# Performance work log

Hardware: AMD Instinct MI355X
Metric: run time of the kernel (lower is better)

## Reference

```python
import jax, jax.numpy as jnp
import numpy as np

N, E, G = 50000, 1600000, 512
IN_DIM, HEADS, C1, C2, HIDDEN = 128, 3, 32, 32, 512
NEG_SLOPE = 0.2
EPS = 1e-16


def _glorot(key, shape):
    fan_in = shape[0]
    return jax.random.normal(key, shape, dtype=jnp.float32) / np.sqrt(fan_in)


def setup_inputs() -> dict:
    key = jax.random.key(0)
    ks = jax.random.split(key, 16)
    x = jax.random.normal(ks[0], (N, IN_DIM), dtype=jnp.float32)
    edge_index = jax.random.randint(ks[1], (2, E), 0, N, dtype=jnp.int64)
    batch = (jnp.arange(N, dtype=jnp.int64) * G) // N  # sorted, all graphs non-empty
    d1, d2 = HEADS * C1, HEADS * C2
    return {
        "x": x,
        "W_l1": _glorot(ks[2], (IN_DIM, d1)), "b_l1": jnp.zeros((d1,), jnp.float32),
        "W_r1": _glorot(ks[3], (IN_DIM, d1)), "b_r1": jnp.zeros((d1,), jnp.float32),
        "att1": _glorot(ks[4], (HEADS, C1)), "bias1": jnp.zeros((d1,), jnp.float32),
        "W_l2": _glorot(ks[5], (d1, d2)), "b_l2": jnp.zeros((d2,), jnp.float32),
        "W_r2": _glorot(ks[6], (d1, d2)), "b_r2": jnp.zeros((d2,), jnp.float32),
        "att2": _glorot(ks[7], (HEADS, C2)), "bias2": jnp.zeros((d2,), jnp.float32),
        "W_fc1": _glorot(ks[8], (d1 + d2, HIDDEN)), "b_fc1": jnp.zeros((HIDDEN,), jnp.float32),
        "W_fc2": _glorot(ks[9], (HIDDEN, 2)), "b_fc2": jnp.zeros((2,), jnp.float32),
        "edge_index": edge_index,
        "batch": batch,
    }


def gatv2_conv(xin, src, dst, W_l, b_l, W_r, b_r, att, bias, heads, out_c):
    n = xin.shape[0]
    x_l = (xin @ W_l + b_l).reshape(n, heads, out_c)  # source-side projection
    x_r = (xin @ W_r + b_r).reshape(n, heads, out_c)  # target-side projection
    e = jax.nn.leaky_relu(x_l[src] + x_r[dst], NEG_SLOPE)  # [E', H, C]
    logits = jnp.einsum("ehc,hc->eh", e, att)  # [E', H]
    m = jax.ops.segment_max(logits, dst, num_segments=n)
    a = jnp.exp(logits - m[dst])
    denom = jax.ops.segment_sum(a, dst, num_segments=n)
    alpha = a / (denom[dst] + EPS)  # per-destination edge softmax (PyG semantics)
    out = jax.ops.segment_sum(x_l[src] * alpha[:, :, None], dst, num_segments=n)
    return out.reshape(n, heads * out_c) + bias


def reference(x, W_l1, b_l1, W_r1, b_r1, att1, bias1,
              W_l2, b_l2, W_r2, b_r2, att2, bias2,
              W_fc1, b_fc1, W_fc2, b_fc2, edge_index, batch):
    n = x.shape[0]
    loop = jnp.arange(n, dtype=edge_index.dtype)
    src = jnp.concatenate([edge_index[0], loop])  # PyG GATv2Conv adds self-loops
    dst = jnp.concatenate([edge_index[1], loop])
    h1 = jnp.tanh(gatv2_conv(x, src, dst, W_l1, b_l1, W_r1, b_r1, att1, bias1, HEADS, C1))
    h2 = jnp.tanh(gatv2_conv(h1, src, dst, W_l2, b_l2, W_r2, b_r2, att2, bias2, HEADS, C2))
    h = jnp.concatenate([h1, h2], axis=1)  # [N, (C1+C2)*H]
    first_idx = jnp.searchsorted(batch, jnp.arange(G, dtype=batch.dtype))  # first node of each graph
    pooled = h[first_idx]  # [G, (C1+C2)*H]
    hidden = jax.nn.relu(pooled @ W_fc1 + b_fc1)
    logits = hidden @ W_fc2 + b_fc2
    return jax.nn.log_softmax(logits, axis=1)
```

## Files before the change

kernel.cpp:

```cpp
#include <hip/hip_runtime.h>
#include <hip/hip_bf16.h>
#include <hip/hip_fp16.h>
#include <math.h>

#define NN 50000
#define EE 1600000
#define GG 512
#define INDIM 128
#define HEADS 3
#define CC 32
#define DD 96
#define HID 512
#define NEG 0.2f
#define NEGM1 (NEG - 1.0f)
#define EPS_DEN 1e-16f
#define CAP 128
#define NBW 1568
#define LOG2E 1.44269504f
#define PCLAMP2 86.5617f

#define PS_BL1   0
#define PS_BR1   96
#define PS_ATT1  192
#define PS_BIAS1 288
#define PS_BL2   384
#define PS_BR2   480
#define PS_ATT2  576
#define PS_BIAS2 672
#define PS_BFC1  768
#define PS_WFC2  1280
#define PS_BFC2  2304
#define PS_TOTAL 2308

typedef _Float16 h8 __attribute__((ext_vector_type(8)));
typedef float f4 __attribute__((ext_vector_type(4)));

static __device__ __forceinline__ float bf2f(__hip_bfloat16 v) { return __bfloat162float(v); }

static __device__ __forceinline__ int getI(const void* p, long long i, bool w64) {
    return w64 ? ((const int*)p)[2 * i] : ((const int*)p)[i];
}

static __device__ __forceinline__ float rawf(const void* p, int i, bool isbf) {
    return isbf ? bf2f(((const __hip_bfloat16*)p)[i]) : ((const float*)p)[i];
}

static __device__ __forceinline__ void load4(const void* p, int base, int e0, bool w64, int* v) {
    const int4* q = (const int4*)p;
    if (w64) {
        int4 a = q[(base + e0) >> 1];
        int4 b = q[((base + e0) >> 1) + 1];
        v[0] = a.x; v[1] = a.z; v[2] = b.x; v[3] = b.z;
    } else {
        int4 a = q[(base + e0) >> 2];
        v[0] = a.x; v[1] = a.y; v[2] = a.z; v[3] = a.w;
    }
}

static __device__ __forceinline__ bool testbit(const unsigned* b, int i) {
    return (b[i >> 5] >> (i & 31)) & 1u;
}

template <int CTRL>
static __device__ __forceinline__ float dpp_add(float v) {
    int t = __builtin_amdgcn_update_dpp(0, __float_as_int(v), CTRL, 0xF, 0xF, true);
    return v + __int_as_float(t);
}
static __device__ __forceinline__ float red16(float p) {
    p = dpp_add<0x121>(p);
    p = dpp_add<0x122>(p);
    p = dpp_add<0x124>(p);
    p = dpp_add<0x128>(p);
    return p;
}

static __device__ __forceinline__ float edge_e(float2 x, float2 xr2, float2 aa) {
    float t0 = x.x + xr2.x; t0 = fmaf(fminf(t0, 0.0f), NEGM1, t0);
    float t1 = x.y + xr2.y; t1 = fmaf(fminf(t1, 0.0f), NEGM1, t1);
    return exp2f(fminf(red16(fmaf(t1, aa.y, t0 * aa.x)), PCLAMP2));
}

__global__ void detect_kernel(const void* __restrict__ x, const void* __restrict__ ei,
                              int* __restrict__ flags)
{
    __shared__ int wild, zcnt;
    if (threadIdx.x == 0) { wild = 0; zcnt = 0; }
    __syncthreads();
    int w = 0, z = 0;
    const __hip_bfloat16* xb = (const __hip_bfloat16*)x;
    for (int i = threadIdx.x; i < 4096; i += 256) {
        float v = bf2f(xb[i]);
        if (!(fabsf(v) <= 1e6f)) w++;
    }
    const int* e32 = (const int*)ei;
    for (int i = threadIdx.x; i < 4096; i += 256) {
        if (e32[2 * i + 1] == 0) z++;
    }
    atomicAdd(&wild, w);
    atomicAdd(&zcnt, z);
    __syncthreads();
    if (threadIdx.x == 0) {
        flags[0] = (wild < 64) ? 1 : 0;
        flags[1] = (zcnt > 4000) ? 1 : 0;
    }
}

struct SetupArgs {
    const void *wl1, *wr1, *wl2, *wr2, *wfc1;
    const void *bl1, *br1, *att1, *bias1, *bl2, *br2, *att2, *bias2, *bfc1, *wfc2, *bfc2;
    const void *batch;
};

__global__ void setup_kernel(SetupArgs a, const int* __restrict__ flags,
                             float* __restrict__ P, __half* __restrict__ B1,
                             __half* __restrict__ B2, __half* __restrict__ Bfc,
                             int* __restrict__ deg, int* __restrict__ needed,
                             int* __restrict__ first, unsigned* __restrict__ pb,
                             int* __restrict__ cnt)
{
    const int task = blockIdx.y;
    const int idx = blockIdx.x * 256 + threadIdx.x;
    const bool isbf = flags[0] != 0;

    if (task == 0) {
        if (idx == 0) *cnt = 0;
        if (idx >= PS_TOTAL) return;
        const void* src; int rel;
        if (idx < 768) {
            int k = idx / 96; rel = idx - k * 96;
            const void* s8[8] = {a.bl1, a.br1, a.att1, a.bias1, a.bl2, a.br2, a.att2, a.bias2};
            src = s8[k];
        } else if (idx < 1280) { src = a.bfc1; rel = idx - 768; }
        else if (idx < 2304)   { src = a.wfc2; rel = idx - 1280; }
        else if (idx < 2306)   { src = a.bfc2; rel = idx - 2304; }
        else return;
        P[idx] = rawf(src, rel, isbf);
    } else if (task == 1 || task == 2) {
        const int KC = (task == 1) ? 4 : 3;
        const int total = 12 * KC * 64;
        if (idx >= total) return;
        int lane = idx & 63, t = idx >> 6;
        int kc = t % KC, ntile = t / KC;
        int n = ntile * 16 + (lane & 15);
        int kbase = kc * 32 + (lane >> 4) * 8;
        const void* W = (task == 1) ? (n < 96 ? a.wl1 : a.wr1) : (n < 96 ? a.wl2 : a.wr2);
        int n2 = (n < 96) ? n : n - 96;
        __half* dst = ((task == 1) ? B1 : B2) + (size_t)idx * 8;
#pragma unroll
        for (int j = 0; j < 8; j++) dst[j] = __float2half(rawf(W, (kbase + j) * 96 + n2, isbf));
    } else if (task == 3) {
        const int total = 32 * 6 * 64;
        if (idx >= total) return;
        int lane = idx & 63, t = idx >> 6;
        int kc = t % 6, ntile = t / 6;
        int n = ntile * 16 + (lane & 15);
        int kbase = kc * 32 + (lane >> 4) * 8;
        __half* dst = Bfc + (size_t)idx * 8;
#pragma unroll
        for (int j = 0; j < 8; j++) dst[j] = __float2half(rawf(a.wfc1, (kbase + j) * HID + n, isbf));
    } else if (task == 4) {
        int i0 = idx * 4;
#pragma unroll
        for (int j = 0; j < 4; j++) if (i0 + j < NN) deg[i0 + j] = 0;
    } else if (task == 5) {
        if (idx >= NN) return;
        const bool w64 = flags[1] != 0;
        int b = getI(a.batch, idx, w64);
        bool isf = (idx == 0) || (getI(a.batch, idx - 1, w64) != b);
        needed[idx] = isf ? 1 : 0;
        if (isf) first[b] = idx;
    } else {
        if (idx >= NBW) return;
        const bool w64 = flags[1] != 0;
        unsigned word = 0;
        int prev = (idx == 0) ? -1 : getI(a.batch, idx * 32 - 1, w64);
        for (int bit = 0; bit < 32; bit++) {
            int i = idx * 32 + bit;
            if (i >= NN) break;
            int b = getI(a.batch, i, w64);
            if (i == 0 || b != prev) word |= (1u << bit);
            prev = b;
        }
        pb[idx] = word;
    }
}

__global__ void mark_needed_kernel(const void* __restrict__ ei, const int* __restrict__ flags,
                                   const unsigned* __restrict__ pb, int* __restrict__ needed)
{
    int e0 = (blockIdx.x * 256 + threadIdx.x) * 4;
    if (e0 >= EE) return;
    const bool w64 = flags[1] != 0;
    int d4[4];
    load4(ei, EE, e0, w64, d4);
#pragma unroll
    for (int j = 0; j < 4; j++)
        if (testbit(pb, d4[j])) needed[getI(ei, e0 + j, w64)] = 1;
}

__global__ void scatter_compact_kernel(const void* __restrict__ ei, const int* __restrict__ flags,
                                       const int* __restrict__ needed,
                                       int* __restrict__ deg, int* __restrict__ csr,
                                       int* __restrict__ list, int* __restrict__ cnt)
{
    if (blockIdx.y == 1) {
        int i = blockIdx.x * 256 + threadIdx.x;
        if (i >= NN) return;
        if (needed[i]) list[atomicAdd(cnt, 1)] = i;
        return;
    }
    int e0 = (blockIdx.x * 256 + threadIdx.x) * 4;
    if (e0 >= EE) return;
    const bool w64 = flags[1] != 0;
    int s4[4], d4[4];
    load4(ei, EE, e0, w64, d4);
    int nd0 = needed[d4[0]], nd1 = needed[d4[1]], nd2 = needed[d4[2]], nd3 = needed[d4[3]];
    if (!(nd0 | nd1 | nd2 | nd3)) return;
    load4(ei, 0, e0, w64, s4);
    int nd[4] = {nd0, nd1, nd2, nd3};
#pragma unroll
    for (int j = 0; j < 4; j++) {
        int dst = d4[j];
        if (!nd[j]) continue;
        int pos = atomicAdd(&deg[dst], 1);
        if (pos < CAP) csr[(size_t)dst * CAP + pos] = s4[j] * (DD / 2);
    }
}

template <int KDIM, int MODE>
__global__ __launch_bounds__(256) void proj_mfma_kernel(
    const void* __restrict__ Ain, const __half* __restrict__ Bswz,
    const int* __restrict__ list, const int* __restrict__ cnt,
    const float* __restrict__ P, const int* __restrict__ flags, int offBl, int offBr,
    __half* __restrict__ xl, float* __restrict__ xr)
{
    constexpr int KC = KDIM / 32;
    __shared__ __half Bs[12 * KC * 64 * 8];
    const int tid = threadIdx.x;
    const int limit = MODE ? *cnt : NN;
    const int blockBase = blockIdx.x * 64;
    if (blockBase >= limit) return;

    {
        const int chunks = 12 * KC * 64;
        for (int i = tid; i < chunks; i += 256)
            reinterpret_cast<f4*>(Bs)[i] = reinterpret_cast<const f4*>(Bswz)[i];
    }
    __syncthreads();

    const int wave = tid >> 6;
    const int lane = tid & 63;
    const int base = blockBase + wave * 16;
    if (base >= limit) return;

    const int q = lane >> 4;
    const int mlane = lane & 15;

    int aIdx = base + mlane;
    int aRow;
    if (MODE) aRow = (aIdx < limit) ? list[aIdx] : list[limit - 1];
    else      aRow = (aIdx < limit) ? aIdx : 0;

    h8 a[KC];
    if (MODE == 1) {
        const h8* arow = reinterpret_cast<const h8*>((const __half*)Ain + (size_t)aRow * KDIM);
#pragma unroll
        for (int kc = 0; kc < KC; kc++) a[kc] = arow[kc * 4 + q];
    } else if (flags[0]) {
        const int4* arow = reinterpret_cast<const int4*>((const ushort*)Ain + (size_t)aRow * KDIM);
#pragma unroll
        for (int kc = 0; kc < KC; kc++) {
            int4 r = arow[kc * 4 + q];
            int ws[4] = {r.x, r.y, r.z, r.w};
#pragma unroll
            for (int i = 0; i < 4; i++) {
                a[kc][2 * i]     = (_Float16)__int_as_float(ws[i] << 16);
                a[kc][2 * i + 1] = (_Float16)__int_as_float(ws[i] & 0xffff0000);
            }
        }
    } else {
        const f4* arow = reinterpret_cast<const f4*>((const float*)Ain + (size_t)aRow * KDIM);
#pragma unroll
        for (int kc = 0; kc < KC; kc++) {
            f4 r0 = arow[kc * 8 + q * 2];
            f4 r1 = arow[kc * 8 + q * 2 + 1];
#pragma unroll
            for (int i = 0; i < 4; i++) {
                a[kc][i]     = (_Float16)r0[i];
                a[kc][4 + i] = (_Float16)r1[i];
            }
        }
    }

    int sRow[4];
#pragma unroll
    for (int r = 0; r < 4; r++) {
        int si = base + q * 4 + r;
        sRow[r] = (si < limit) ? (MODE ? list[si] : si) : -1;
    }

    const h8* Bf = reinterpret_cast<const h8*>(Bs);
#pragma unroll
    for (int ntile = 0; ntile < 12; ntile++) {
        int n = ntile * 16 + mlane;
        float bv = (n < 96) ? P[offBl + n] : P[offBr + n - 96];
        f4 acc = {bv, bv, bv, bv};
#pragma unroll
        for (int kc = 0; kc < KC; kc++) {
            h8 b = Bf[(ntile * KC + kc) * 64 + lane];
            acc = __builtin_amdgcn_mfma_f32_16x16x32_f16(a[kc], b, acc, 0, 0, 0);
        }
#pragma unroll
        for (int r = 0; r < 4; r++) {
            if (sRow[r] < 0) continue;
            if (n < 96) xl[(size_t)sRow[r] * DD + n] = __float2half(acc[r]);
            else        xr[(size_t)sRow[r] * DD + (n - 96)] = acc[r];
        }
    }
}

template <int OUTMODE>
__global__ __launch_bounds__(256) void fused_edge_kernel(
    const int* __restrict__ csr, const int* __restrict__ deg,
    const int* __restrict__ list, const int* __restrict__ cnt,
    const __half* __restrict__ xl, const float* __restrict__ xr,
    const float* __restrict__ P, int offAtt, int offBias,
    __half* __restrict__ out)
{
    const int lane = threadIdx.x & 63;
    const int g = lane >> 4;
    const int t = lane & 15;
    const int w0 = (blockIdx.x * 256 + threadIdx.x) >> 6;
    const int nw = (gridDim.x * 256) >> 6;
    const int limit = (OUTMODE == 0) ? *cnt : GG;
    const __half2* xl2p = reinterpret_cast<const __half2*>(xl);

    float2 a_[3];
#pragma unroll
    for (int h = 0; h < 3; h++) {
        float2 av = *reinterpret_cast<const float2*>(P + offAtt + h * CC + 2 * t);
        a_[h].x = av.x * LOG2E; a_[h].y = av.y * LOG2E;
    }

    for (int li = w0; li < limit; li += nw) {
        const int n = list[li];
        const int* row = csr + (size_t)n * CAP;
        const int end = min(deg[n], CAP);
        const float* xrn = xr + (size_t)n * DD;
        float2 xr_[3];
#pragma unroll
        for (int h = 0; h < 3; h++) xr_[h] = *reinterpret_cast<const float2*>(xrn + h * CC + 2 * t);

        float d0, d1, d2, o00, o01, o10, o11, o20, o21;
        {
            const __half2* sp = xl2p + n * (DD / 2) + t;
            float2 x0 = __half22float2(sp[0]);
            float2 x1 = __half22float2(sp[16]);
            float2 x2 = __half22float2(sp[32]);
            float e0 = edge_e(x0, xr_[0], a_[0]);
            float e1 = edge_e(x1, xr_[1], a_[1]);
            float e2 = edge_e(x2, xr_[2], a_[2]);
            if (g == 0) {
                d0 = e0; o00 = e0 * x0.x; o01 = e0 * x0.y;
                d1 = e1; o10 = e1 * x1.x; o11 = e1 * x1.y;
                d2 = e2; o20 = e2 * x2.x; o21 = e2 * x2.y;
            } else {
                d0 = d1 = d2 = 0.0f;
                o00 = o01 = o10 = o11 = o20 = o21 = 0.0f;
            }
        }

        int k = g;
        for (; k + 12 < end; k += 16) {
            int s0 = row[k], s1 = row[k + 4], s2 = row[k + 8], s3 = row[k + 12];
            const __half2* p0 = xl2p + s0 + t;
            const __half2* p1 = xl2p + s1 + t;
            const __half2* p2 = xl2p + s2 + t;
            const __half2* p3 = xl2p + s3 + t;
            __half2 r00 = p0[0], r01 = p0[16], r02 = p0[32];
            __half2 r10 = p1[0], r11 = p1[16], r12 = p1[32];
            __half2 r20 = p2[0], r21 = p2[16], r22 = p2[32];
            __half2 r30 = p3[0], r31 = p3[16], r32 = p3[32];
            float2 xa0 = __half22float2(r00), xa1 = __half22float2(r01), xa2 = __half22float2(r02);
            float2 xb0 = __half22float2(r10), xb1 = __half22float2(r11), xb2 = __half22float2(r12);
            float2 xc0 = __half22float2(r20), xc1 = __half22float2(r21), xc2 = __half22float2(r22);
            float2 xd0 = __half22float2(r30), xd1 = __half22float2(r31), xd2 = __half22float2(r32);
            float ea0 = edge_e(xa0, xr_[0], a_[0]), ea1 = edge_e(xa1, xr_[1], a_[1]), ea2 = edge_e(xa2, xr_[2], a_[2]);
            float eb0 = edge_e(xb0, xr_[0], a_[0]), eb1 = edge_e(xb1, xr_[1], a_[1]), eb2 = edge_e(xb2, xr_[2], a_[2]);
            float ec0 = edge_e(xc0, xr_[0], a_[0]), ec1 = edge_e(xc1, xr_[1], a_[1]), ec2 = edge_e(xc2, xr_[2], a_[2]);
            float ed0 = edge_e(xd0, xr_[0], a_[0]), ed1 = edge_e(xd1, xr_[1], a_[1]), ed2 = edge_e(xd2, xr_[2], a_[2]);
            d0 += (ea0 + eb0) + (ec0 + ed0);
            d1 += (ea1 + eb1) + (ec1 + ed1);
            d2 += (ea2 + eb2) + (ec2 + ed2);
            o00 = fmaf(ea0, xa0.x, o00); o00 = fmaf(eb0, xb0.x, o00); o00 = fmaf(ec0, xc0.x, o00); o00 = fmaf(ed0, xd0.x, o00);
            o01 = fmaf(ea0, xa0.y, o01); o01 = fmaf(eb0, xb0.y, o01); o01 = fmaf(ec0, xc0.y, o01); o01 = fmaf(ed0, xd0.y, o01);
            o10 = fmaf(ea1, xa1.x, o10); o10 = fmaf(eb1, xb1.x, o10); o10 = fmaf(ec1, xc1.x, o10); o10 = fmaf(ed1, xd1.x, o10);
            o11 = fmaf(ea1, xa1.y, o11); o11 = fmaf(eb1, xb1.y, o11); o11 = fmaf(ec1, xc1.y, o11); o11 = fmaf(ed1, xd1.y, o11);
            o20 = fmaf(ea2, xa2.x, o20); o20 = fmaf(eb2, xb2.x, o20); o20 = fmaf(ec2, xc2.x, o20); o20 = fmaf(ed2, xd2.x, o20);
            o21 = fmaf(ea2, xa2.y, o21); o21 = fmaf(eb2, xb2.y, o21); o21 = fmaf(ec2, xc2.y, o21); o21 = fmaf(ed2, xd2.y, o21);
        }
        for (; k + 4 < end; k += 8) {
            int s0 = row[k], s1 = row[k + 4];
            const __half2* p0 = xl2p + s0 + t;
            const __half2* p1 = xl2p + s1 + t;
            __half2 ra0 = p0[0], ra1 = p0[16], ra2 = p0[32];
            __half2 rb0 = p1[0], rb1 = p1[16], rb2 = p1[32];
            float2 xa0 = __half22float2(ra0), xa1 = __half22float2(ra1), xa2 = __half22float2(ra2);
            float2 xb0 = __half22float2(rb0), xb1 = __half22float2(rb1), xb2 = __half22float2(rb2);
            float ea0 = edge_e(xa0, xr_[0], a_[0]), ea1 = edge_e(xa1, xr_[1], a_[1]), ea2 = edge_e(xa2, xr_[2], a_[2]);
            float eb0 = edge_e(xb0, xr_[0], a_[0]), eb1 = edge_e(xb1, xr_[1], a_[1]), eb2 = edge_e(xb2, xr_[2], a_[2]);
            d0 += ea0 + eb0; d1 += ea1 + eb1; d2 += ea2 + eb2;
            o00 = fmaf(ea0, xa0.x, o00); o00 = fmaf(eb0, xb0.x, o00);
            o01 = fmaf(ea0, xa0.y, o01); o01 = fmaf(eb0, xb0.y, o01);
            o10 = fmaf(ea1, xa1.x, o10); o10 = fmaf(eb1, xb1.x, o10);
            o11 = fmaf(ea1, xa1.y, o11); o11 = fmaf(eb1, xb1.y, o11);
            o20 = fmaf(ea2, xa2.x, o20); o20 = fmaf(eb2, xb2.x, o20);
            o21 = fmaf(ea2, xa2.y, o21); o21 = fmaf(eb2, xb2.y, o21);
        }
        for (; k < end; k += 4) {
            int s0 = row[k];
            const __half2* p0 = xl2p + s0 + t;
            float2 xa0 = __half22float2(p0[0]);
            float2 xa1 = __half22float2(p0[16]);
            float2 xa2 = __half22float2(p0[32]);
            float ea0 = edge_e(xa0, xr_[0], a_[0]);
            float ea1 = edge_e(xa1, xr_[1], a_[1]);
            float ea2 = edge_e(xa2, xr_[2], a_[2]);
            d0 += ea0; d1 += ea1; d2 += ea2;
            o00 = fmaf(ea0, xa0.x, o00); o01 = fmaf(ea0, xa0.y, o01);
            o10 = fmaf(ea1, xa1.x, o10); o11 = fmaf(ea1, xa1.y, o11);
            o20 = fmaf(ea2, xa2.x, o20); o21 = fmaf(ea2, xa2.y, o21);
        }

        d0 += __shfl_xor(d0, 16); d0 += __shfl_xor(d0, 32);
        d1 += __shfl_xor(d1, 16); d1 += __shfl_xor(d1, 32);
        d2 += __shfl_xor(d2, 16); d2 += __shfl_xor(d2, 32);
        o00 += __shfl_xor(o00, 16); o00 += __shfl_xor(o00, 32);
        o01 += __shfl_xor(o01, 16); o01 += __shfl_xor(o01, 32);
        o10 += __shfl_xor(o10, 16); o10 += __shfl_xor(o10, 32);
        o11 += __shfl_xor(o11, 16); o11 += __shfl_xor(o11, 32);
        o20 += __shfl_xor(o20, 16); o20 += __shfl_xor(o20, 32);
        o21 += __shfl_xor(o21, 16); o21 += __shfl_xor(o21, 32);

        if (g == 0) {
            float inv0 = 1.0f / (d0 + EPS_DEN);
            float inv1 = 1.0f / (d1 + EPS_DEN);
            float inv2 = 1.0f / (d2 + EPS_DEN);
            float2 bv0 = *reinterpret_cast<const float2*>(P + offBias + 0 * CC + 2 * t);
            float2 bv1 = *reinterpret_cast<const float2*>(P + offBias + 1 * CC + 2 * t);
            float2 bv2 = *reinterpret_cast<const float2*>(P + offBias + 2 * CC + 2 * t);
            __half2 h0 = __floats2half2_rn(tanhf(fmaf(o00, inv0, bv0.x)), tanhf(fmaf(o01, inv0, bv0.y)));
            __half2 h1 = __floats2half2_rn(tanhf(fmaf(o10, inv1, bv1.x)), tanhf(fmaf(o11, inv1, bv1.y)));
            __half2 h2 = __floats2half2_rn(tanhf(fmaf(o20, inv2, bv2.x)), tanhf(fmaf(o21, inv2, bv2.y)));
            __half* ob = (OUTMODE == 0) ? (out + (size_t)n * DD) : (out + (size_t)li * DD);
            *reinterpret_cast<__half2*>(ob + 0 * CC + 2 * t) = h0;
            *reinterpret_cast<__half2*>(ob + 1 * CC + 2 * t) = h1;
            *reinterpret_cast<__half2*>(ob + 2 * CC + 2 * t) = h2;
        }
    }
}

__global__ __launch_bounds__(256) void mlp_mfma_kernel(
    const __half* __restrict__ h1h, const __half* __restrict__ A2,
    const int* __restrict__ first, const __half* __restrict__ Bfc,
    const float* __restrict__ P, const int* __restrict__ flags, void* __restrict__ outv)
{
    const int tid = threadIdx.x;
    const int wave = tid >> 6, lane = tid & 63;
    const int q = lane >> 4, ml = lane & 15;
    const int rowbase = blockIdx.x * 64 + wave * 16;
    const int g16 = rowbase + ml;

    h8 a[6];
    {
        const h8* l = reinterpret_cast<const h8*>(h1h + (size_t)first[g16] * DD);
#pragma unroll
        for (int kc = 0; kc < 3; kc++) a[kc] = l[kc * 4 + q];
        const h8* r = reinterpret_cast<const h8*>(A2 + (size_t)g16 * DD);
#pragma unroll
        for (int kc = 3; kc < 6; kc++) a[kc] = r[(kc - 3) * 4 + q];
    }

    const h8* Bf = reinterpret_cast<const h8*>(Bfc);
    const float* w2 = P + PS_WFC2;
    float p0[4] = {0, 0, 0, 0}, p1[4] = {0, 0, 0, 0};
    for (int nt = 0; nt < 32; nt++) {
        int n = nt * 16 + ml;
        float bv = P[PS_BFC1 + n];
        f4 acc = {bv, bv, bv, bv};
#pragma unroll
        for (int kc = 0; kc < 6; kc++)
            acc = __builtin_amdgcn_mfma_f32_16x16x32_f16(a[kc], Bf[(nt * 6 + kc) * 64 + lane], acc, 0, 0, 0);
        float w20 = w2[2 * n], w21 = w2[2 * n + 1];
#pragma unroll
        for (int r = 0; r < 4; r++) {
            float hdn = fmaxf(acc[r], 0.0f);
            p0[r] = fmaf(hdn, w20, p0[r]);
            p1[r] = fmaf(hdn, w21, p1[r]);
        }
    }
#pragma unroll
    for (int off = 1; off <= 8; off <<= 1) {
#pragma unroll
        for (int r = 0; r < 4; r++) {
            p0[r] += __shfl_xor(p0[r], off);
            p1[r] += __shfl_xor(p1[r], off);
        }
    }
    if (ml == 0) {
        float b0 = P[PS_BFC2], b1 = P[PS_BFC2 + 1];
#pragma unroll
        for (int r = 0; r < 4; r++) {
            int g = rowbase + q * 4 + r;
            float l0 = p0[r] + b0, l1 = p1[r] + b1;
            float mx = fmaxf(l0, l1);
            float lse = mx + logf(__expf(l0 - mx) + __expf(l1 - mx));
            if (flags[0]) {
                ((__hip_bfloat16*)outv)[g * 2 + 0] = __float2bfloat16(l0 - lse);
                ((__hip_bfloat16*)outv)[g * 2 + 1] = __float2bfloat16(l1 - lse);
            } else {
                ((float*)outv)[g * 2 + 0] = l0 - lse;
                ((float*)outv)[g * 2 + 1] = l1 - lse;
            }
        }
    }
}

extern "C" void kernel_launch(void* const* d_in, const int* in_sizes, int n_in,
                              void* d_out, int out_size, void* d_ws, size_t ws_size,
                              hipStream_t stream)
{
    const void* x     = d_in[0];
    const void* ei    = d_in[17];
    const void* batch = d_in[18];

    float* ws   = (float*)d_ws;
    float* P    = ws;
    float* xr   = P + PS_TOTAL;

    __half* hp   = (__half*)(xr + (size_t)NN * DD);
    __half* xlh  = hp;
    __half* xl2h = xlh + (size_t)NN * DD;
    __half* h1h  = xl2h + (size_t)NN * DD;
    __half* A2   = h1h + (size_t)NN * DD;
    __half* B1   = A2 + (size_t)GG * DD;
    __half* B2   = B1 + 24576;
    __half* Bfc  = B2 + 18432;

    int* ip       = (int*)(Bfc + 98304);
    int* deg      = ip;
    int* needed   = deg + NN;
    int* cnt      = needed + NN;
    int* csr      = cnt + 4;
    int* list     = csr + (size_t)NN * CAP;
    int* first    = list + NN;
    int* flags    = first + GG;
    unsigned* pb  = (unsigned*)(flags + 4);

    SetupArgs sa;
    sa.wl1 = d_in[1];  sa.bl1 = d_in[2];  sa.wr1 = d_in[3];  sa.br1 = d_in[4];
    sa.att1 = d_in[5]; sa.bias1 = d_in[6];
    sa.wl2 = d_in[7];  sa.bl2 = d_in[8];  sa.wr2 = d_in[9];  sa.br2 = d_in[10];
    sa.att2 = d_in[11]; sa.bias2 = d_in[12];
    sa.wfc1 = d_in[13]; sa.bfc1 = d_in[14]; sa.wfc2 = d_in[15]; sa.bfc2 = d_in[16];
    sa.batch = batch;

    const int edge4B = (EE / 4 + 255) / 256;
    const int mprojB = (NN + 63) / 64;
    const int fuse1B = 2048;
    const int fuse2B = GG / 4;

    detect_kernel<<<1, 256, 0, stream>>>(x, ei, flags);
    setup_kernel<<<dim3(196, 7), 256, 0, stream>>>(sa, flags, P, B1, B2, Bfc,
                                                   deg, needed, first, pb, cnt);
    mark_needed_kernel<<<edge4B, 256, 0, stream>>>(ei, flags, pb, needed);
    scatter_compact_kernel<<<dim3(edge4B, 2), 256, 0, stream>>>(ei, flags, needed,
                                                                deg, csr, list, cnt);

    proj_mfma_kernel<INDIM, 0><<<mprojB, 256, 0, stream>>>(x, B1, nullptr, nullptr,
                                                           P, flags, PS_BL1, PS_BR1, xlh, xr);
    fused_edge_kernel<0><<<fuse1B, 256, 0, stream>>>(csr, deg, list, cnt, xlh, xr,
                                                     P, PS_ATT1, PS_BIAS1, h1h);

    proj_mfma_kernel<DD, 1><<<mprojB, 256, 0, stream>>>(h1h, B2, list, cnt,
                                                        P, flags, PS_BL2, PS_BR2, xl2h, xr);
    fused_edge_kernel<1><<<fuse2B, 256, 0, stream>>>(csr, deg, first, nullptr, xl2h, xr,
                                                     P, PS_ATT2, PS_BIAS2, A2);

    mlp_mfma_kernel<<<GG / 64, 256, 0, stream>>>(h1h, A2, first, Bfc, P, flags, d_out);
}
```

Baseline: 259.8 us.

## Fuse layer-1 projection into scatter/compact kernel and read weights from global

The layer-1 node projection becomes a third grid slice of the edge scatter/compact kernel, so it runs alongside the CSR build in one launch and one kernel boundary disappears. The projection body is factored into a device function that reads the swizzled weight fragments straight from global memory. The shared-memory staging and its barrier are gone. This overlaps independent work and cuts launch and sync cost, but each wave now reads weights through the cache hierarchy instead of LDS. The combined kernel also launches many idle projection blocks, since its x-dimension is sized for the edge slice.

```diff
diff --git a/kernel.cpp b/kernel.cpp
--- a/kernel.cpp
+++ b/kernel.cpp
@@ -198,12 +198,102 @@
         if (testbit(pb, d4[j])) needed[getI(ei, e0 + j, w64)] = 1;
 }
 
-__global__ void scatter_compact_kernel(const void* __restrict__ ei, const int* __restrict__ flags,
-                                       const int* __restrict__ needed,
-                                       int* __restrict__ deg, int* __restrict__ csr,
-                                       int* __restrict__ list, int* __restrict__ cnt)
-{
-    if (blockIdx.y == 1) {
+template <int KDIM, int MODE>
+static __device__ __forceinline__ void proj_body(
+    int bx, const void* __restrict__ Ain, const __half* __restrict__ Bg,
+    const int* __restrict__ list, const int* __restrict__ cnt,
+    const float* __restrict__ P, const int* __restrict__ flags, int offBl, int offBr,
+    __half* __restrict__ xl, float* __restrict__ xr)
+{
+    constexpr int KC = KDIM / 32;
+    const int tid = threadIdx.x;
+    const int limit = MODE ? *cnt : NN;
+    const int wave = tid >> 6;
+    const int lane = tid & 63;
+    const int base = bx * 64 + wave * 16;
+    if (base >= limit) return;
+
+    const int q = lane >> 4;
+    const int mlane = lane & 15;
+
+    int aIdx = base + mlane;
+    int aRow;
+    if (MODE) aRow = (aIdx < limit) ? list[aIdx] : list[limit - 1];
+    else      aRow = (aIdx < limit) ? aIdx : 0;
+
+    h8 a[KC];
+    if (MODE == 1) {
+        const h8* arow = reinterpret_cast<const h8*>((const __half*)Ain + (size_t)aRow * KDIM);
+#pragma unroll
+        for (int kc = 0; kc < KC; kc++) a[kc] = arow[kc * 4 + q];
+    } else if (flags[0]) {
+        const int4* arow = reinterpret_cast<const int4*>((const ushort*)Ain + (size_t)aRow * KDIM);
+#pragma unroll
+        for (int kc = 0; kc < KC; kc++) {
+            int4 r = arow[kc * 4 + q];
+            int ws[4] = {r.x, r.y, r.z, r.w};
+#pragma unroll
+            for (int i = 0; i < 4; i++) {
+                a[kc][2 * i]     = (_Float16)__int_as_float(ws[i] << 16);
+                a[kc][2 * i + 1] = (_Float16)__int_as_float(ws[i] & 0xffff0000);
+            }
+        }
+    } else {
+        const f4* arow = reinterpret_cast<const f4*>((const float*)Ain + (size_t)aRow * KDIM);
+#pragma unroll
+        for (int kc = 0; kc < KC; kc++) {
+            f4 r0 = arow[kc * 8 + q * 2];
+            f4 r1 = arow[kc * 8 + q * 2 + 1];
+#pragma unroll
+            for (int i = 0; i < 4; i++) {
+                a[kc][i]     = (_Float16)r0[i];
+                a[kc][4 + i] = (_Float16)r1[i];
+            }
+        }
+    }
+
+    int sRow[4];
+#pragma unroll
+    for (int r = 0; r < 4; r++) {
+        int si = base + q * 4 + r;
+        sRow[r] = (si < limit) ? (MODE ? list[si] : si) : -1;
+    }
+
+    const h8* Bf = reinterpret_cast<const h8*>(Bg);
+#pragma unroll
+    for (int ntile = 0; ntile < 12; ntile++) {
+        int n = ntile * 16 + mlane;
+        float bv = (n < 96) ? P[offBl + n] : P[offBr + n - 96];
+        f4 acc = {bv, bv, bv, bv};
+#pragma unroll
+        for (int kc = 0; kc < KC; kc++) {
+            h8 b = Bf[(ntile * KC + kc) * 64 + lane];
+            acc = __builtin_amdgcn_mfma_f32_16x16x32_f16(a[kc], b, acc, 0, 0, 0);
+        }
+#pragma unroll
+        for (int r = 0; r < 4; r++) {
+            if (sRow[r] < 0) continue;
+            if (n < 96) xl[(size_t)sRow[r] * DD + n] = __float2half(acc[r]);
+            else        xr[(size_t)sRow[r] * DD + (n - 96)] = acc[r];
+        }
+    }
+}
+
+__global__ __launch_bounds__(256) void mid_kernel(
+    const void* __restrict__ ei, const int* __restrict__ flags,
+    const int* __restrict__ needed,
+    int* __restrict__ deg, int* __restrict__ csr,
+    int* __restrict__ list, int* __restrict__ cnt,
+    const void* __restrict__ x, const __half* __restrict__ B1,
+    const float* __restrict__ P, __half* __restrict__ xl, float* __restrict__ xr)
+{
+    const int slice = blockIdx.y;
+    if (slice == 2) {
+        proj_body<INDIM, 0>(blockIdx.x, x, B1, nullptr, nullptr, P, flags,
+                            PS_BL1, PS_BR1, xl, xr);
+        return;
+    }
+    if (slice == 1) {
         int i = blockIdx.x * 256 + threadIdx.x;
         if (i >= NN) return;
         if (needed[i]) list[atomicAdd(cnt, 1)] = i;
@@ -228,95 +318,13 @@
 }
 
 template <int KDIM, int MODE>
-__global__ __launch_bounds__(256) void proj_mfma_kernel(
-    const void* __restrict__ Ain, const __half* __restrict__ Bswz,
+__global__ __launch_bounds__(256) void proj_g_kernel(
+    const void* __restrict__ Ain, const __half* __restrict__ Bg,
     const int* __restrict__ list, const int* __restrict__ cnt,
     const float* __restrict__ P, const int* __restrict__ flags, int offBl, int offBr,
     __half* __restrict__ xl, float* __restrict__ xr)
 {
-    constexpr int KC = KDIM / 32;
-    __shared__ __half Bs[12 * KC * 64 * 8];
-    const int tid = threadIdx.x;
-    const int limit = MODE ? *cnt : NN;
-    const int blockBase = blockIdx.x * 64;
-    if (blockBase >= limit) return;
-
-    {
-        const int chunks = 12 * KC * 64;
-        for (int i = tid; i < chunks; i += 256)
-            reinterpret_cast<f4*>(Bs)[i] = reinterpret_cast<const f4*>(Bswz)[i];
-    }
-    __syncthreads();
-
-    const int wave = tid >> 6;
-    const int lane = tid & 63;
-    const int base = blockBase + wave * 16;
-    if (base >= limit) return;
-
-    const int q = lane >> 4;
-    const int mlane = lane & 15;
-
-    int aIdx = base + mlane;
-    int aRow;
-    if (MODE) aRow = (aIdx < limit) ? list[aIdx] : list[limit - 1];
-    else      aRow = (aIdx < limit) ? aIdx : 0;
-
-    h8 a[KC];
-    if (MODE == 1) {
-        const h8* arow = reinterpret_cast<const h8*>((const __half*)Ain + (size_t)aRow * KDIM);
-#pragma unroll
-        for (int kc = 0; kc < KC; kc++) a[kc] = arow[kc * 4 + q];
-    } else if (flags[0]) {
-        const int4* arow = reinterpret_cast<const int4*>((const ushort*)Ain + (size_t)aRow * KDIM);
-#pragma unroll
-        for (int kc = 0; kc < KC; kc++) {
-            int4 r = arow[kc * 4 + q];
-            int ws[4] = {r.x, r.y, r.z, r.w};
-#pragma unroll
-            for (int i = 0; i < 4; i++) {
-                a[kc][2 * i]     = (_Float16)__int_as_float(ws[i] << 16);
-                a[kc][2 * i + 1] = (_Float16)__int_as_float(ws[i] & 0xffff0000);
-            }
-        }
-    } else {
-        const f4* arow = reinterpret_cast<const f4*>((const float*)Ain + (size_t)aRow * KDIM);
-#pragma unroll
-        for (int kc = 0; kc < KC; kc++) {
-            f4 r0 = arow[kc * 8 + q * 2];
-            f4 r1 = arow[kc * 8 + q * 2 + 1];
-#pragma unroll
-            for (int i = 0; i < 4; i++) {
-                a[kc][i]     = (_Float16)r0[i];
-                a[kc][4 + i] = (_Float16)r1[i];
-            }
-        }
-    }
-
-    int sRow[4];
-#pragma unroll
-    for (int r = 0; r < 4; r++) {
-        int si = base + q * 4 + r;
-        sRow[r] = (si < limit) ? (MODE ? list[si] : si) : -1;
-    }
-
-    const h8* Bf = reinterpret_cast<const h8*>(Bs);
-#pragma unroll
-    for (int ntile = 0; ntile < 12; ntile++) {
-        int n = ntile * 16 + mlane;
-        float bv = (n < 96) ? P[offBl + n] : P[offBr + n - 96];
-        f4 acc = {bv, bv, bv, bv};
-#pragma unroll
-        for (int kc = 0; kc < KC; kc++) {
-            h8 b = Bf[(ntile * KC + kc) * 64 + lane];
-            acc = __builtin_amdgcn_mfma_f32_16x16x32_f16(a[kc], b, acc, 0, 0, 0);
-        }
-#pragma unroll
-        for (int r = 0; r < 4; r++) {
-            if (sRow[r] < 0) continue;
-            if (n < 96) xl[(size_t)sRow[r] * DD + n] = __float2half(acc[r]);
-            else        xr[(size_t)sRow[r] * DD + (n - 96)] = acc[r];
-        }
-    }
+    proj_body<KDIM, MODE>(blockIdx.x, Ain, Bg, list, cnt, P, flags, offBl, offBr, xl, xr);
 }
 
 template <int OUTMODE>
@@ -574,16 +582,15 @@
     setup_kernel<<<dim3(196, 7), 256, 0, stream>>>(sa, flags, P, B1, B2, Bfc,
                                                    deg, needed, first, pb, cnt);
     mark_needed_kernel<<<edge4B, 256, 0, stream>>>(ei, flags, pb, needed);
-    scatter_compact_kernel<<<dim3(edge4B, 2), 256, 0, stream>>>(ei, flags, needed,
-                                                                deg, csr, list, cnt);
-
-    proj_mfma_kernel<INDIM, 0><<<mprojB, 256, 0, stream>>>(x, B1, nullptr, nullptr,
-                                                           P, flags, PS_BL1, PS_BR1, xlh, xr);
+
+    mid_kernel<<<dim3(edge4B, 3), 256, 0, stream>>>(ei, flags, needed, deg, csr, list, cnt,
+                                                    x, B1, P, xlh, xr);
+
     fused_edge_kernel<0><<<fuse1B, 256, 0, stream>>>(csr, deg, list, cnt, xlh, xr,
                                                      P, PS_ATT1, PS_BIAS1, h1h);
 
-    proj_mfma_kernel<DD, 1><<<mprojB, 256, 0, stream>>>(h1h, B2, list, cnt,
-                                                        P, flags, PS_BL2, PS_BR2, xl2h, xr);
+    proj_g_kernel<DD, 1><<<mprojB, 256, 0, stream>>>(h1h, B2, list, cnt,
+                                                     P, flags, PS_BL2, PS_BR2, xl2h, xr);
     fused_edge_kernel<1><<<fuse2B, 256, 0, stream>>>(csr, deg, first, nullptr, xl2h, xr,
                                                      P, PS_ATT2, PS_BIAS2, A2);
 
```

After: 254.0 us. 1.02x faster.
